# Optimization experiments

Hardware: AMD Instinct MI355X
Metric: run time of the kernel (lower is better)

Reference implementation:

```python
import jax, jax.numpy as jnp
import numpy as np

N_HEAD, D_MODEL, D_HEAD = 16, 1024, 64
QLEN, MLEN, BATCH = 1024, 1024, 4
KLEN = QLEN + MLEN
LN_EPS = 1e-5


def _rel_shift(x):
    # x: [q, r, b, n] -> Transformer-XL relative shift
    q, r = x.shape[0], x.shape[1]
    zero_pad = jnp.zeros((q, 1) + x.shape[2:], x.dtype)
    x_padded = jnp.concatenate([zero_pad, x], axis=1)  # [q, r+1, b, n]
    x_padded = x_padded.reshape((r + 1, q) + x.shape[2:])
    return x_padded[1:].reshape(x.shape)


def _layer_norm(x, gamma, beta):
    mu = jnp.mean(x, axis=-1, keepdims=True)
    var = jnp.var(x, axis=-1, keepdims=True)
    return (x - mu) * jax.lax.rsqrt(var + LN_EPS) * gamma + beta


def setup_inputs() -> dict:
    key = jax.random.key(0)
    ks = jax.random.split(key, 10)
    d, n, dh = D_MODEL, N_HEAD, D_HEAD
    content = jax.random.normal(ks[0], (QLEN, BATCH, d), jnp.float32)
    mems = jax.random.normal(ks[1], (MLEN, BATCH, d), jnp.float32)
    rel_pos = jax.random.normal(ks[2], (KLEN, d), jnp.float32)
    r_w_bias = jax.random.normal(ks[3], (n, dh), jnp.float32) * 0.02
    r_r_bias = jax.random.normal(ks[4], (n, dh), jnp.float32) * 0.02
    s = 1.0 / np.sqrt(d)
    W_qkv = jax.random.normal(ks[5], (d, 3 * n * dh), jnp.float32) * s
    W_r = jax.random.normal(ks[6], (d, n * dh), jnp.float32) * s
    W_o = jax.random.normal(ks[7], (n * dh, d), jnp.float32) * s
    ln_gamma = jnp.ones((d,), jnp.float32)
    ln_beta = jnp.zeros((d,), jnp.float32)
    # causal mask with memory: query i attends to keys j <= i + MLEN (True = masked)
    attn_mask = jnp.arange(KLEN)[None, :] > (jnp.arange(QLEN)[:, None] + MLEN)
    return {
        "content": content, "rel_pos": rel_pos, "mems": mems,
        "r_w_bias": r_w_bias, "r_r_bias": r_r_bias,
        "W_qkv": W_qkv, "W_r": W_r, "W_o": W_o,
        "ln_gamma": ln_gamma, "ln_beta": ln_beta,
        "attn_mask": attn_mask,
    }


def reference(content, rel_pos, mems, r_w_bias, r_r_bias, W_qkv, W_r, W_o, ln_gamma, ln_beta, attn_mask):
    qlen, b = content.shape[0], content.shape[1]
    n, dh = N_HEAD, D_HEAD
    scale = 1.0 / np.sqrt(dh)

    cat = jnp.concatenate([mems, content], axis=0)            # [klen, b, d]
    klen = cat.shape[0]
    w_heads = cat @ W_qkv                                     # [klen, b, 3*n*dh]
    w_q, w_k, w_v = jnp.split(w_heads, 3, axis=-1)
    w_q = w_q[-qlen:].reshape(qlen, b, n, dh)
    w_k = w_k.reshape(klen, b, n, dh)
    w_v = w_v.reshape(klen, b, n, dh)
    r_k = (rel_pos @ W_r).reshape(-1, n, dh)                  # [rlen, n, dh]

    AC = jnp.einsum('ibnd,jbnd->ijbn', w_q + r_w_bias, w_k)
    BD = _rel_shift(jnp.einsum('ibnd,jnd->ijbn', w_q + r_r_bias, r_k))
    attn_score = (AC + BD) * scale                            # [q, k, b, n]
    attn_score = jnp.where(attn_mask[:, :, None, None], -jnp.inf, attn_score)
    attn_prob = jax.nn.softmax(attn_score, axis=1)

    attn_vec = jnp.einsum('ijbn,jbnd->ibnd', attn_prob, w_v)
    attn_vec = attn_vec.reshape(qlen, b, n * dh)
    attn_out = attn_vec @ W_o                                 # [q, b, d]
    return _layer_norm(content + attn_out, ln_gamma, ln_beta)
```

## Files before the change

kernel.cpp:

```cpp
#include <hip/hip_runtime.h>

#define QLEN 1024
#define MLEN 1024
#define KLEN 2048
#define BATCH 4
#define NHEAD 16
#define DHEAD 64
#define DMODEL 1024

typedef _Float16 half8 __attribute__((ext_vector_type(8)));
typedef _Float16 half4 __attribute__((ext_vector_type(4)));
typedef float f32x4 __attribute__((ext_vector_type(4)));

#define NEG_INF (-__builtin_inff())
#define QSCALE 0.18033688011112042f

typedef __attribute__((address_space(3))) unsigned int lds_u32;
typedef __attribute__((address_space(1))) unsigned int glb_u32;

__device__ __forceinline__ void gll16(void* lds, const void* g) {
  __builtin_amdgcn_global_load_lds((const glb_u32*)g, (lds_u32*)lds, 16, 0, 0);
}

__global__ __launch_bounds__(256) void k_pack_cat(const float* __restrict__ mems,
                                                  const float* __restrict__ content,
                                                  _Float16* __restrict__ Acat)
{
  int idx = blockIdx.x * 256 + threadIdx.x;
  int e = idx * 4;
  int m = e >> 10, kk = e & 1023;
  int crow = m >> 2, bb = m & 3;
  const float* src;
  if (crow < MLEN) src = mems + (size_t)(crow * BATCH + bb) * DMODEL + kk;
  else             src = content + (size_t)((crow - MLEN) * BATCH + bb) * DMODEL + kk;
  float4 v = *(const float4*)src;
  half4 o = { (_Float16)v.x, (_Float16)v.y, (_Float16)v.z, (_Float16)v.w };
  *(half4*)(Acat + (size_t)m * DMODEL + kk) = o;
}

__global__ __launch_bounds__(256) void k_prep(const float* __restrict__ Wqkv,
                                              const float* __restrict__ Wr,
                                              const float* __restrict__ Wo,
                                              const float* __restrict__ rel_pos,
                                              _Float16* __restrict__ WqkvT,
                                              _Float16* __restrict__ WrT,
                                              _Float16* __restrict__ WoT,
                                              _Float16* __restrict__ RelP)
{
  __shared__ float T[64][65];
  const int z = blockIdx.z;
  const int tid = threadIdx.x;
  if (z == 3) {
    int nb = gridDim.x * gridDim.y;
    int bid = blockIdx.y * gridDim.x + blockIdx.x;
    for (int e = (bid * 256 + tid) * 4; e < KLEN * DMODEL; e += nb * 256 * 4) {
      float4 v = *(const float4*)(rel_pos + e);
      half4 o = { (_Float16)v.x, (_Float16)v.y, (_Float16)v.z, (_Float16)v.w };
      *(half4*)(RelP + e) = o;
    }
    return;
  }
  const float* in; _Float16* out; int C;
  if (z == 0)      { in = Wqkv; out = WqkvT; C = 3072; }
  else if (z == 1) { if (blockIdx.x >= 16) return; in = Wr; out = WrT; C = 1024; }
  else             { if (blockIdx.x >= 16) return; in = Wo; out = WoT; C = 1024; }
  const int R = 1024;
  int c0 = blockIdx.x * 64, r0 = blockIdx.y * 64;
#pragma unroll
  for (int u = 0; u < 16; ++u) {
    int lin = u * 256 + tid;
    int rr = lin >> 6, cc = lin & 63;
    T[rr][cc] = in[(size_t)(r0 + rr) * C + c0 + cc];
  }
  __syncthreads();
#pragma unroll
  for (int u = 0; u < 16; ++u) {
    int lin = u * 256 + tid;
    int cc = lin >> 6, rr = lin & 63;
    out[(size_t)(c0 + cc) * R + r0 + rr] = (_Float16)T[rr][cc];
  }
}

__global__ __launch_bounds__(256) void k_trans_v(const _Float16* __restrict__ Vb,
                                                 _Float16* __restrict__ VbT)
{
  __shared__ _Float16 T[64][72];
  int r0 = blockIdx.x * 64;
  int bh = blockIdx.y;
  const _Float16* in = Vb + (size_t)bh * KLEN * DHEAD;
  _Float16* out = VbT + (size_t)bh * DHEAD * KLEN;
  int tid = threadIdx.x;
#pragma unroll
  for (int u = 0; u < 16; ++u) {
    int lin = u * 256 + tid;
    int rr = lin >> 6, cc = lin & 63;
    T[rr][cc] = in[(size_t)(r0 + rr) * DHEAD + cc];
  }
  __syncthreads();
#pragma unroll
  for (int u = 0; u < 16; ++u) {
    int lin = u * 256 + tid;
    int cc = lin >> 6, rr = lin & 63;
    out[(size_t)cc * KLEN + r0 + rr] = T[rr][cc];
  }
}

template<typename Epi>
__device__ __forceinline__ void gemm_tile_128(const _Float16* __restrict__ A,
                                              const _Float16* __restrict__ B,
                                              int K, Epi epi)
{
  __shared__ __align__(16) _Float16 As[128 * 32];
  __shared__ __align__(16) _Float16 Bs[128 * 32];
  const int tid = threadIdx.x;
  const int lane = tid & 63;
  const int wave = tid >> 6;
  const int q = lane >> 4, l16 = lane & 15;
  const int wm = wave >> 1, wn = wave & 1;
  const int m0 = blockIdx.y * 128, n0 = blockIdx.x * 128;
  f32x4 acc[4][4] = {};

  for (int k0 = 0; k0 < K; k0 += 32) {
    __syncthreads();
#pragma unroll
    for (int i = 0; i < 2; ++i) {
      int c = i * 256 + tid;
      int row = c >> 2, pos = c & 3;
      int col8 = pos ^ ((row >> 1) & 3);
      gll16(&As[c * 8], A + (size_t)(m0 + row) * K + k0 + col8 * 8);
      gll16(&Bs[c * 8], B + (size_t)(n0 + row) * K + k0 + col8 * 8);
    }
    __syncthreads();
    half8 a[4], b[4];
#pragma unroll
    for (int rt = 0; rt < 4; ++rt) {
      int row = wm * 64 + rt * 16 + l16;
      a[rt] = *(const half8*)&As[(row * 4 + (q ^ ((row >> 1) & 3))) * 8];
    }
#pragma unroll
    for (int ct = 0; ct < 4; ++ct) {
      int row = wn * 64 + ct * 16 + l16;
      b[ct] = *(const half8*)&Bs[(row * 4 + (q ^ ((row >> 1) & 3))) * 8];
    }
#pragma unroll
    for (int rt = 0; rt < 4; ++rt)
#pragma unroll
      for (int ct = 0; ct < 4; ++ct)
        acc[rt][ct] = __builtin_amdgcn_mfma_f32_16x16x32_f16(a[rt], b[ct], acc[rt][ct], 0, 0, 0);
  }
#pragma unroll
  for (int rt = 0; rt < 4; ++rt)
#pragma unroll
    for (int ct = 0; ct < 4; ++ct)
#pragma unroll
      for (int reg = 0; reg < 4; ++reg) {
        int m = m0 + wm * 64 + rt * 16 + q * 4 + reg;
        int nn = n0 + wn * 64 + ct * 16 + l16;
        epi(m, nn, acc[rt][ct][reg]);
      }
}

__global__ __launch_bounds__(256, 2) void k_gemm_qkv(
    const _Float16* __restrict__ A, const _Float16* __restrict__ B,
    _Float16* __restrict__ Qw, _Float16* __restrict__ Qr,
    _Float16* __restrict__ Kb, _Float16* __restrict__ Vb,
    const float* __restrict__ rwb, const float* __restrict__ rrb)
{
  if (blockIdx.x < 8 && blockIdx.y < 32) return;
  const int sec = blockIdx.x >> 3;
  gemm_tile_128(A, B, DMODEL, [=](int m, int nn, float v) {
    int c = nn & 1023;
    int hh = c >> 6, dd = c & 63;
    int crow = m >> 2, bb = m & 3;
    int bhh = bb * NHEAD + hh;
    if (sec == 0) {
      int i = crow - MLEN;
      size_t o = ((size_t)bhh * QLEN + i) * DHEAD + dd;
      Qw[o] = (_Float16)((v + rwb[c]) * QSCALE);
      Qr[o] = (_Float16)((v + rrb[c]) * QSCALE);
    } else if (sec == 1) {
      Kb[((size_t)bhh * KLEN + crow) * DHEAD + dd] = (_Float16)v;
    } else {
      Vb[((size_t)bhh * KLEN + crow) * DHEAD + dd] = (_Float16)v;
    }
  });
}

__global__ __launch_bounds__(256, 2) void k_gemm_rk(
    const _Float16* __restrict__ A, const _Float16* __restrict__ B,
    _Float16* __restrict__ Rk2)
{
  gemm_tile_128(A, B, DMODEL, [=](int m, int nn, float v) {
    int hh = nn >> 6, dd = nn & 63;
    Rk2[((size_t)hh * KLEN + m) * DHEAD + dd] = (_Float16)v;
  });
}

__global__ __launch_bounds__(256, 2) void k_gemm_out(
    const _Float16* __restrict__ A, const _Float16* __restrict__ B,
    const float* __restrict__ content, float* __restrict__ Y)
{
  gemm_tile_128(A, B, DMODEL, [=](int m, int nn, float v) {
    Y[(size_t)m * DMODEL + nn] = v + content[(size_t)m * DMODEL + nn];
  });
}

__global__ __launch_bounds__(256, 4) void k_attn(
    const _Float16* __restrict__ Qw, const _Float16* __restrict__ Qr,
    const _Float16* __restrict__ Kb, const _Float16* __restrict__ VbT,
    const _Float16* __restrict__ Rk2, _Float16* __restrict__ AV)
{
  __shared__ __align__(16) _Float16 Kl[2][64 * 64];
  __shared__ __align__(16) _Float16 Vtl[2][64 * 64];
  __shared__ __align__(16) _Float16 Pl[4][16 * 64];

  const int tid = threadIdx.x;
  const int lane = tid & 63, wave = tid >> 6;
  const int q = lane >> 4, l16 = lane & 15;
  const int i0 = (15 - blockIdx.x) * 64;
  const int bh = blockIdx.y;
  const int h = bh & 15, bb = bh >> 4;

  const _Float16* Qwb = Qw + (size_t)bh * QLEN * DHEAD;
  const _Float16* Qrb = Qr + (size_t)bh * QLEN * DHEAD;
  const _Float16* Kbb = Kb + (size_t)bh * KLEN * DHEAD;
  const _Float16* Vtb = VbT + (size_t)bh * DHEAD * KLEN;
  const _Float16* Rkb = Rk2 + (size_t)h * KLEN * DHEAD;

  const int iw = i0 + wave * 16;

  half8 aqw[2], aqr[2];
#pragma unroll
  for (int s = 0; s < 2; ++s) {
    size_t o = (size_t)(iw + l16) * DHEAD + s * 32 + q * 8;
    aqw[s] = *(const half8*)(Qwb + o);
    aqr[s] = *(const half8*)(Qrb + o);
  }

  f32x4 oa[4] = {};
  float l_lane[4] = {};
  _Float16* Plw = &Pl[wave][0];

  auto stage = [&](int j0s, int bufi) {
#pragma unroll
    for (int i = 0; i < 2; ++i) {
      int c = i * 256 + tid;
      int row = c >> 3;
      int col8 = (c & 7) ^ (row & 7);
      gll16(&Kl[bufi][c * 8],  Kbb + (size_t)(j0s + row) * DHEAD + col8 * 8);
      gll16(&Vtl[bufi][c * 8], Vtb + (size_t)row * KLEN + j0s + col8 * 8);
    }
  };

  const int n_jt = (i0 >> 6) + 17;
  stage(0, 0);
  for (int jt = 0; jt < n_jt; ++jt) {
    const int j0 = jt * 64;
    const int bufi = jt & 1;
    __syncthreads();
    if (jt + 1 < n_jt) stage((jt + 1) * 64, bufi ^ 1);

    if (j0 > iw + 15 + MLEN) continue;
    const _Float16* Klb = Kl[bufi];
    const _Float16* Vtlb = Vtl[bufi];

    const int rs = j0 - iw + 1008;
    half8 rk_a[2], rk_b[2];
    {
      int r = rs + l16;
      int rc = r < 0 ? 0 : (r > KLEN - 1 ? KLEN - 1 : r);
      const _Float16* base = Rkb + (size_t)rc * DHEAD + q * 8;
      rk_a[0] = *(const half8*)(base);
      rk_a[1] = *(const half8*)(base + 32);
    }

    f32x4 ac[4] = {};
#pragma unroll
    for (int ct = 0; ct < 4; ++ct) {
      int row = ct * 16 + l16;
#pragma unroll
      for (int s = 0; s < 2; ++s) {
        int pos = (s * 4 + q) ^ (row & 7);
        half8 bk = *(const half8*)&Klb[(row * 8 + pos) * 8];
        ac[ct] = __builtin_amdgcn_mfma_f32_16x16x32_f16(aqw[s], bk, ac[ct], 0, 0, 0);
      }
    }

    f32x4 bd[5] = {};
#pragma unroll
    for (int rt = 0; rt < 5; ++rt) {
      if (rt + 1 < 5) {
        int r = rs + (rt + 1) * 16 + l16;
        int rc = r < 0 ? 0 : (r > KLEN - 1 ? KLEN - 1 : r);
        const _Float16* base = Rkb + (size_t)rc * DHEAD + q * 8;
        half8 (&nxt)[2] = (rt & 1) ? rk_a : rk_b;
        nxt[0] = *(const half8*)(base);
        nxt[1] = *(const half8*)(base + 32);
      }
      half8 (&cur)[2] = (rt & 1) ? rk_b : rk_a;
      bd[rt] = __builtin_amdgcn_mfma_f32_16x16x32_f16(aqr[0], cur[0], bd[rt], 0, 0, 0);
      bd[rt] = __builtin_amdgcn_mfma_f32_16x16x32_f16(aqr[1], cur[1], bd[rt], 0, 0, 0);
    }

    const bool boundary = (j0 + 63 > iw + MLEN);
#pragma unroll
    for (int reg = 0; reg < 4; ++reg) {
      const int m = q * 4 + reg;
      const int src = (l16 + 15 - m) & 15;
      float sh[5];
#pragma unroll
      for (int rt = 0; rt < 5; ++rt) sh[rt] = __shfl(bd[rt][reg], src, 16);
      const bool sel = (l16 > m);
      float acc = 0.f;
#pragma unroll
      for (int ct = 0; ct < 4; ++ct) {
        float bdv = sel ? sh[ct + 1] : sh[ct];
        float sv = ac[ct][reg] + bdv;
        if (boundary && (j0 + ct * 16 + l16 > iw + m + MLEN)) sv = NEG_INF;
        float e = __builtin_amdgcn_exp2f(sv);
        acc += e;
        int c = ct * 16 + l16;
        Plw[m * 64 + (((c >> 3) ^ (m & 7)) * 8) + (c & 7)] = (_Float16)e;
      }
      l_lane[reg] += acc;
    }

    half8 ap[2];
#pragma unroll
    for (int s = 0; s < 2; ++s)
      ap[s] = *(const half8*)&Plw[l16 * 64 + (((s * 4 + q) ^ (l16 & 7)) * 8)];
#pragma unroll
    for (int t = 0; t < 4; ++t) {
      int row = t * 16 + l16;
#pragma unroll
      for (int s = 0; s < 2; ++s) {
        int pos = (s * 4 + q) ^ (row & 7);
        half8 bv = *(const half8*)&Vtlb[(row * 8 + pos) * 8];
        oa[t] = __builtin_amdgcn_mfma_f32_16x16x32_f16(ap[s], bv, oa[t], 0, 0, 0);
      }
    }
  }

  float linv[4];
#pragma unroll
  for (int reg = 0; reg < 4; ++reg) {
    float v = l_lane[reg];
    v += __shfl_xor(v, 1, 16);
    v += __shfl_xor(v, 2, 16);
    v += __shfl_xor(v, 4, 16);
    v += __shfl_xor(v, 8, 16);
    linv[reg] = 1.0f / v;
  }
#pragma unroll
  for (int t = 0; t < 4; ++t)
#pragma unroll
    for (int reg = 0; reg < 4; ++reg) {
      int ii = iw + q * 4 + reg;
      AV[(size_t)(ii * BATCH + bb) * DMODEL + h * DHEAD + t * 16 + l16] =
          (_Float16)(oa[t][reg] * linv[reg]);
    }
}

__global__ __launch_bounds__(256) void k_ln(const float* __restrict__ Y,
                                            const float* __restrict__ gamma,
                                            const float* __restrict__ beta,
                                            float* __restrict__ out)
{
  int row = blockIdx.x, tid = threadIdx.x;
  const float4 v = ((const float4*)(Y + (size_t)row * DMODEL))[tid];
  float s = v.x + v.y + v.z + v.w;
  float ss = v.x * v.x + v.y * v.y + v.z * v.z + v.w * v.w;
#pragma unroll
  for (int off = 32; off >= 1; off >>= 1) {
    s += __shfl_xor(s, off, 64);
    ss += __shfl_xor(ss, off, 64);
  }
  __shared__ float red[8];
  int wave = tid >> 6, lane = tid & 63;
  if (lane == 0) { red[wave] = s; red[4 + wave] = ss; }
  __syncthreads();
  s = red[0] + red[1] + red[2] + red[3];
  ss = red[4] + red[5] + red[6] + red[7];
  float mu = s * (1.0f / DMODEL);
  float var = ss * (1.0f / DMODEL) - mu * mu;
  float rstd = rsqrtf(var + 1e-5f);
  const float4 g = ((const float4*)gamma)[tid];
  const float4 bt = ((const float4*)beta)[tid];
  float4 o;
  o.x = (v.x - mu) * rstd * g.x + bt.x;
  o.y = (v.y - mu) * rstd * g.y + bt.y;
  o.z = (v.z - mu) * rstd * g.z + bt.z;
  o.w = (v.w - mu) * rstd * g.w + bt.w;
  ((float4*)(out + (size_t)row * DMODEL))[tid] = o;
}

extern "C" void kernel_launch(void* const* d_in, const int* in_sizes, int n_in,
                              void* d_out, int out_size, void* d_ws, size_t ws_size,
                              hipStream_t stream)
{
  (void)in_sizes; (void)n_in; (void)out_size; (void)ws_size;
  const float* content = (const float*)d_in[0];
  const float* rel_pos = (const float*)d_in[1];
  const float* mems    = (const float*)d_in[2];
  const float* rwb     = (const float*)d_in[3];
  const float* rrb     = (const float*)d_in[4];
  const float* Wqkv    = (const float*)d_in[5];
  const float* Wr      = (const float*)d_in[6];
  const float* Wo      = (const float*)d_in[7];
  const float* gamma   = (const float*)d_in[8];
  const float* beta    = (const float*)d_in[9];

  char* ws = (char*)d_ws;
  size_t off = 0;
  auto take = [&](size_t bytes) { char* p = ws + off; off += (bytes + 255) & ~(size_t)255; return p; };

  _Float16* Acat  = (_Float16*)take(8192ull * 1024 * 2);
  _Float16* WqkvT = (_Float16*)take(3072ull * 1024 * 2);
  _Float16* RelP  = (_Float16*)take(2048ull * 1024 * 2);
  _Float16* WrT   = (_Float16*)take(1024ull * 1024 * 2);
  _Float16* WoT   = (_Float16*)take(1024ull * 1024 * 2);
  _Float16* Qw    = (_Float16*)take(64ull * 1024 * 64 * 2);
  _Float16* Qr    = (_Float16*)take(64ull * 1024 * 64 * 2);
  _Float16* Kb    = (_Float16*)take(64ull * 2048 * 64 * 2);
  _Float16* Vb    = (_Float16*)take(64ull * 2048 * 64 * 2);
  _Float16* AV    = (_Float16*)take(4096ull * 1024 * 2);
  _Float16* VbT   = Acat;
  _Float16* Rk2   = WqkvT;
  float*    Y     = (float*)Kb;
  float*    out   = (float*)d_out;

  k_pack_cat<<<dim3(8192), dim3(256), 0, stream>>>(mems, content, Acat);
  k_prep<<<dim3(48, 16, 4), dim3(256), 0, stream>>>(Wqkv, Wr, Wo, rel_pos, WqkvT, WrT, WoT, RelP);
  k_gemm_qkv<<<dim3(24, 64), dim3(256), 0, stream>>>(Acat, WqkvT, Qw, Qr, Kb, Vb, rwb, rrb);
  k_gemm_rk<<<dim3(8, 16), dim3(256), 0, stream>>>(RelP, WrT, Rk2);
  k_trans_v<<<dim3(32, 64), dim3(256), 0, stream>>>(Vb, VbT);
  k_attn<<<dim3(16, 64), dim3(256), 0, stream>>>(Qw, Qr, Kb, VbT, Rk2, AV);
  k_gemm_out<<<dim3(8, 32), dim3(256), 0, stream>>>(AV, WoT, content, Y);
  k_ln<<<dim3(4096), dim3(256), 0, stream>>>(Y, gamma, beta, out);
}
```

Measured before the change: 436.1 us.

## Merge pack into prep, fuse QKV and Rk GEMMs, prefetch Rk before staging

Folds the mems/content fp16 pack into the prep kernel as an extra z-slice, and merges the R_k projection GEMM into the QKV GEMM launch as extra block rows, so two launches and their serialization gaps disappear. Rk2 gets its own workspace buffer because it can no longer alias WqkvT while both GEMMs run concurrently. In attention, all five R_k fragments are loaded up front before the next K/V tile is staged, trading a software double-buffer for more registers in flight. This adds register pressure in k_attn and uses a larger grid of partly idle blocks in the fused GEMM.

Measured after the change: 583.0 us. 33.7% more time.

```diff
diff --git a/kernel.cpp b/kernel.cpp
--- a/kernel.cpp
+++ b/kernel.cpp
@@ -22,30 +22,17 @@
   __builtin_amdgcn_global_load_lds((const glb_u32*)g, (lds_u32*)lds, 16, 0, 0);
 }
 
-__global__ __launch_bounds__(256) void k_pack_cat(const float* __restrict__ mems,
-                                                  const float* __restrict__ content,
-                                                  _Float16* __restrict__ Acat)
-{
-  int idx = blockIdx.x * 256 + threadIdx.x;
-  int e = idx * 4;
-  int m = e >> 10, kk = e & 1023;
-  int crow = m >> 2, bb = m & 3;
-  const float* src;
-  if (crow < MLEN) src = mems + (size_t)(crow * BATCH + bb) * DMODEL + kk;
-  else             src = content + (size_t)((crow - MLEN) * BATCH + bb) * DMODEL + kk;
-  float4 v = *(const float4*)src;
-  half4 o = { (_Float16)v.x, (_Float16)v.y, (_Float16)v.z, (_Float16)v.w };
-  *(half4*)(Acat + (size_t)m * DMODEL + kk) = o;
-}
-
 __global__ __launch_bounds__(256) void k_prep(const float* __restrict__ Wqkv,
                                               const float* __restrict__ Wr,
                                               const float* __restrict__ Wo,
                                               const float* __restrict__ rel_pos,
+                                              const float* __restrict__ mems,
+                                              const float* __restrict__ content,
                                               _Float16* __restrict__ WqkvT,
                                               _Float16* __restrict__ WrT,
                                               _Float16* __restrict__ WoT,
-                                              _Float16* __restrict__ RelP)
+                                              _Float16* __restrict__ RelP,
+                                              _Float16* __restrict__ Acat)
 {
   __shared__ float T[64][65];
   const int z = blockIdx.z;
@@ -60,6 +47,21 @@
     }
     return;
   }
+  if (z == 4) {
+    int nb = gridDim.x * gridDim.y;
+    int bid = blockIdx.y * gridDim.x + blockIdx.x;
+    for (int e = (bid * 256 + tid) * 4; e < 8192 * DMODEL; e += nb * 256 * 4) {
+      int m = e >> 10, kk = e & 1023;
+      int crow = m >> 2, bb = m & 3;
+      const float* src;
+      if (crow < MLEN) src = mems + (size_t)(crow * BATCH + bb) * DMODEL + kk;
+      else             src = content + (size_t)((crow - MLEN) * BATCH + bb) * DMODEL + kk;
+      float4 v = *(const float4*)src;
+      half4 o = { (_Float16)v.x, (_Float16)v.y, (_Float16)v.z, (_Float16)v.w };
+      *(half4*)(Acat + (size_t)m * DMODEL + kk) = o;
+    }
+    return;
+  }
   const float* in; _Float16* out; int C;
   if (z == 0)      { in = Wqkv; out = WqkvT; C = 3072; }
   else if (z == 1) { if (blockIdx.x >= 16) return; in = Wr; out = WrT; C = 1024; }
@@ -108,16 +110,14 @@
 template<typename Epi>
 __device__ __forceinline__ void gemm_tile_128(const _Float16* __restrict__ A,
                                               const _Float16* __restrict__ B,
-                                              int K, Epi epi)
-{
-  __shared__ __align__(16) _Float16 As[128 * 32];
-  __shared__ __align__(16) _Float16 Bs[128 * 32];
+                                              int K, int m0, int n0,
+                                              _Float16* As, _Float16* Bs, Epi epi)
+{
   const int tid = threadIdx.x;
   const int lane = tid & 63;
   const int wave = tid >> 6;
   const int q = lane >> 4, l16 = lane & 15;
   const int wm = wave >> 1, wn = wave & 1;
-  const int m0 = blockIdx.y * 128, n0 = blockIdx.x * 128;
   f32x4 acc[4][4] = {};
 
   for (int k0 = 0; k0 < K; k0 += 32) {
@@ -160,49 +160,57 @@
       }
 }
 
-__global__ __launch_bounds__(256, 2) void k_gemm_qkv(
+__global__ __launch_bounds__(256, 2) void k_gemm_qkv_rk(
     const _Float16* __restrict__ A, const _Float16* __restrict__ B,
+    const _Float16* __restrict__ RelP, const _Float16* __restrict__ WrT,
     _Float16* __restrict__ Qw, _Float16* __restrict__ Qr,
     _Float16* __restrict__ Kb, _Float16* __restrict__ Vb,
+    _Float16* __restrict__ Rk2,
     const float* __restrict__ rwb, const float* __restrict__ rrb)
 {
-  if (blockIdx.x < 8 && blockIdx.y < 32) return;
-  const int sec = blockIdx.x >> 3;
-  gemm_tile_128(A, B, DMODEL, [=](int m, int nn, float v) {
-    int c = nn & 1023;
-    int hh = c >> 6, dd = c & 63;
-    int crow = m >> 2, bb = m & 3;
-    int bhh = bb * NHEAD + hh;
-    if (sec == 0) {
-      int i = crow - MLEN;
-      size_t o = ((size_t)bhh * QLEN + i) * DHEAD + dd;
-      Qw[o] = (_Float16)((v + rwb[c]) * QSCALE);
-      Qr[o] = (_Float16)((v + rrb[c]) * QSCALE);
-    } else if (sec == 1) {
-      Kb[((size_t)bhh * KLEN + crow) * DHEAD + dd] = (_Float16)v;
-    } else {
-      Vb[((size_t)bhh * KLEN + crow) * DHEAD + dd] = (_Float16)v;
-    }
-  });
-}
-
-__global__ __launch_bounds__(256, 2) void k_gemm_rk(
-    const _Float16* __restrict__ A, const _Float16* __restrict__ B,
-    _Float16* __restrict__ Rk2)
-{
-  gemm_tile_128(A, B, DMODEL, [=](int m, int nn, float v) {
-    int hh = nn >> 6, dd = nn & 63;
-    Rk2[((size_t)hh * KLEN + m) * DHEAD + dd] = (_Float16)v;
-  });
+  __shared__ __align__(16) _Float16 As[128 * 32];
+  __shared__ __align__(16) _Float16 Bs[128 * 32];
+  const int bx = blockIdx.x, by = blockIdx.y;
+  if (by >= 64) {
+    if (bx >= 8) return;
+    gemm_tile_128(RelP, WrT, DMODEL, (by - 64) * 128, bx * 128, As, Bs,
+      [=](int m, int nn, float v) {
+        int hh = nn >> 6, dd = nn & 63;
+        Rk2[((size_t)hh * KLEN + m) * DHEAD + dd] = (_Float16)v;
+      });
+    return;
+  }
+  if (bx < 8 && by < 32) return;
+  const int sec = bx >> 3;
+  gemm_tile_128(A, B, DMODEL, by * 128, bx * 128, As, Bs,
+    [=](int m, int nn, float v) {
+      int c = nn & 1023;
+      int hh = c >> 6, dd = c & 63;
+      int crow = m >> 2, bb = m & 3;
+      int bhh = bb * NHEAD + hh;
+      if (sec == 0) {
+        int i = crow - MLEN;
+        size_t o = ((size_t)bhh * QLEN + i) * DHEAD + dd;
+        Qw[o] = (_Float16)((v + rwb[c]) * QSCALE);
+        Qr[o] = (_Float16)((v + rrb[c]) * QSCALE);
+      } else if (sec == 1) {
+        Kb[((size_t)bhh * KLEN + crow) * DHEAD + dd] = (_Float16)v;
+      } else {
+        Vb[((size_t)bhh * KLEN + crow) * DHEAD + dd] = (_Float16)v;
+      }
+    });
 }
 
 __global__ __launch_bounds__(256, 2) void k_gemm_out(
     const _Float16* __restrict__ A, const _Float16* __restrict__ B,
     const float* __restrict__ content, float* __restrict__ Y)
 {
-  gemm_tile_128(A, B, DMODEL, [=](int m, int nn, float v) {
-    Y[(size_t)m * DMODEL + nn] = v + content[(size_t)m * DMODEL + nn];
-  });
+  __shared__ __align__(16) _Float16 As[128 * 32];
+  __shared__ __align__(16) _Float16 Bs[128 * 32];
+  gemm_tile_128(A, B, DMODEL, blockIdx.y * 128, blockIdx.x * 128, As, Bs,
+    [=](int m, int nn, float v) {
+      Y[(size_t)m * DMODEL + nn] = v + content[(size_t)m * DMODEL + nn];
+    });
 }
 
 __global__ __launch_bounds__(256, 4) void k_attn(
@@ -228,6 +236,7 @@
   const _Float16* Rkb = Rk2 + (size_t)h * KLEN * DHEAD;
 
   const int iw = i0 + wave * 16;
+  const int lim = iw + 15 + MLEN;
 
   half8 aqw[2], aqr[2];
 #pragma unroll
@@ -258,21 +267,25 @@
     const int j0 = jt * 64;
     const int bufi = jt & 1;
     __syncthreads();
+
+    const bool act = (j0 <= lim);
+    half8 rk[5][2];
+    if (act) {
+      const int rs = j0 - iw + 1008;
+#pragma unroll
+      for (int rt = 0; rt < 5; ++rt) {
+        int r = rs + rt * 16 + l16;
+        int rc = r < 0 ? 0 : (r > KLEN - 1 ? KLEN - 1 : r);
+        const _Float16* base = Rkb + (size_t)rc * DHEAD + q * 8;
+        rk[rt][0] = *(const half8*)(base);
+        rk[rt][1] = *(const half8*)(base + 32);
+      }
+    }
     if (jt + 1 < n_jt) stage((jt + 1) * 64, bufi ^ 1);
-
-    if (j0 > iw + 15 + MLEN) continue;
+    if (!act) continue;
+
     const _Float16* Klb = Kl[bufi];
     const _Float16* Vtlb = Vtl[bufi];
-
-    const int rs = j0 - iw + 1008;
-    half8 rk_a[2], rk_b[2];
-    {
-      int r = rs + l16;
-      int rc = r < 0 ? 0 : (r > KLEN - 1 ? KLEN - 1 : r);
-      const _Float16* base = Rkb + (size_t)rc * DHEAD + q * 8;
-      rk_a[0] = *(const half8*)(base);
-      rk_a[1] = *(const half8*)(base + 32);
-    }
 
     f32x4 ac[4] = {};
 #pragma unroll
@@ -289,17 +302,8 @@
     f32x4 bd[5] = {};
 #pragma unroll
     for (int rt = 0; rt < 5; ++rt) {
-      if (rt + 1 < 5) {
-        int r = rs + (rt + 1) * 16 + l16;
-        int rc = r < 0 ? 0 : (r > KLEN - 1 ? KLEN - 1 : r);
-        const _Float16* base = Rkb + (size_t)rc * DHEAD + q * 8;
-        half8 (&nxt)[2] = (rt & 1) ? rk_a : rk_b;
-        nxt[0] = *(const half8*)(base);
-        nxt[1] = *(const half8*)(base + 32);
-      }
-      half8 (&cur)[2] = (rt & 1) ? rk_b : rk_a;
-      bd[rt] = __builtin_amdgcn_mfma_f32_16x16x32_f16(aqr[0], cur[0], bd[rt], 0, 0, 0);
-      bd[rt] = __builtin_amdgcn_mfma_f32_16x16x32_f16(aqr[1], cur[1], bd[rt], 0, 0, 0);
+      bd[rt] = __builtin_amdgcn_mfma_f32_16x16x32_f16(aqr[0], rk[rt][0], bd[rt], 0, 0, 0);
+      bd[rt] = __builtin_amdgcn_mfma_f32_16x16x32_f16(aqr[1], rk[rt][1], bd[rt], 0, 0, 0);
     }
 
     const bool boundary = (j0 + 63 > iw + MLEN);
@@ -424,15 +428,15 @@
   _Float16* Kb    = (_Float16*)take(64ull * 2048 * 64 * 2);
   _Float16* Vb    = (_Float16*)take(64ull * 2048 * 64 * 2);
   _Float16* AV    = (_Float16*)take(4096ull * 1024 * 2);
+  _Float16* Rk2   = (_Float16*)take(16ull * 2048 * 64 * 2);
   _Float16* VbT   = Acat;
-  _Float16* Rk2   = WqkvT;
   float*    Y     = (float*)Kb;
   float*    out   = (float*)d_out;
 
-  k_pack_cat<<<dim3(8192), dim3(256), 0, stream>>>(mems, content, Acat);
-  k_prep<<<dim3(48, 16, 4), dim3(256), 0, stream>>>(Wqkv, Wr, Wo, rel_pos, WqkvT, WrT, WoT, RelP);
-  k_gemm_qkv<<<dim3(24, 64), dim3(256), 0, stream>>>(Acat, WqkvT, Qw, Qr, Kb, Vb, rwb, rrb);
-  k_gemm_rk<<<dim3(8, 16), dim3(256), 0, stream>>>(RelP, WrT, Rk2);
+  k_prep<<<dim3(48, 16, 5), dim3(256), 0, stream>>>(Wqkv, Wr, Wo, rel_pos, mems, content,
+                                                    WqkvT, WrT, WoT, RelP, Acat);
+  k_gemm_qkv_rk<<<dim3(24, 80), dim3(256), 0, stream>>>(Acat, WqkvT, RelP, WrT,
+                                                        Qw, Qr, Kb, Vb, Rk2, rwb, rrb);
   k_trans_v<<<dim3(32, 64), dim3(256), 0, stream>>>(Vb, VbT);
   k_attn<<<dim3(16, 64), dim3(256), 0, stream>>>(Qw, Qr, Kb, VbT, Rk2, AV);
   k_gemm_out<<<dim3(8, 32), dim3(256), 0, stream>>>(AV, WoT, content, Y);
```
